# Performance work log

Hardware: AMD Instinct MI355X
Metric: run time of the kernel (lower is better)

Reference implementation:

```python
import jax, jax.numpy as jnp
import numpy as np
from jax import lax

PATCH = 16
DILATIONS = (1, 2, 4, 8)
R2_THRESH = 0.5


def setup_inputs() -> dict:
    key = jax.random.key(0)
    k1, k2, k3 = jax.random.split(key, 3)
    seasonal = jax.random.normal(k1, (32, 2048, 8), dtype=jnp.float32)
    # 4 Conv1d(1,1,k=16) kernels + biases (PyTorch default init scale ~1/sqrt(k))
    conv_w = jax.random.normal(k2, (4, PATCH), dtype=jnp.float32) / np.sqrt(PATCH).astype(np.float32)
    conv_b = jax.random.normal(k3, (4,), dtype=jnp.float32) * 0.01
    return {"seasonal": seasonal, "conv_w": conv_w, "conv_b": conv_b}


def _r2(y):
    n = y.shape[-1]
    x = jnp.arange(n, dtype=y.dtype)
    xm = x - x.mean()                                  # [2p]
    ym = y - y.mean(axis=-1, keepdims=True)            # [..., 2p]
    sxy = jnp.einsum('...k,k->...', ym, xm)
    sxx = jnp.sum(xm * xm)
    syy = jnp.sum(ym * ym, axis=-1)
    return (sxy * sxy) / (sxx * syy)


def _forward(seasonal, conv_w, conv_b):
    B, S, C = seasonal.shape
    p = PATCH
    # channels are processed independently with the SAME convs -> fuse B and C
    x = seasonal.transpose(0, 2, 1).reshape(B * C, 1, S)  # [BC,1,S]
    win = jnp.arange(S - p + 1)[:, None] + jnp.arange(p)[None, :]  # [n_patches,p]
    cand_list = []
    for i, d in enumerate(DILATIONS):
        pad = (p - 1) * d
        out = lax.conv_general_dilated(
            x, conv_w[i].reshape(1, 1, p), window_strides=(1,),
            padding=[(pad, pad)], rhs_dilation=(d,)) + conv_b[i]
        out = out[:, 0, :S]                      # crop to seq_len, [BC,S]
        cand_list.append(out[:, win])            # sliding windows [BC,n_patches,p]
    cand = jnp.concatenate(cand_list, axis=1)    # [BC,N,p]
    N = cand.shape[1]

    # r^2 score for every adjacent pair (vectorized; greedy scan only gates it)
    pair = jnp.concatenate([cand[:, :-1], cand[:, 1:]], axis=-1)  # [BC,N-1,2p]
    can_merge = jnp.pad(_r2(pair) >= R2_THRESH, ((0, 0), (0, 1)),
                        constant_values=False)   # [BC,N]; last idx never merges

    # greedy sequential merge: if pair (i,i+1) merges, i+1 is consumed
    def step(consumed, cm_i):
        merge = jnp.logical_and(~consumed, cm_i)
        return merge, (merge, ~consumed)

    def scan_one(cm):
        _, (merge, valid) = lax.scan(step, jnp.zeros((), jnp.bool_), cm)
        return merge, valid

    merge, valid = jax.vmap(scan_one)(can_merge)  # [BC,N] each

    nxt = jnp.concatenate([cand[:, 1:], cand[:, -1:]], axis=1)
    outs = jnp.where(merge[..., None], 0.5 * (cand + nxt), cand)  # [BC,N,p]

    # pack selected patches to the front (stable order), zero-pad the tail
    order = jnp.argsort(~valid, axis=1)  # jax argsort is stable; valid first
    packed = jnp.take_along_axis(outs, order[..., None], axis=1)
    vmask = jnp.take_along_axis(valid, order, axis=1)
    packed = packed * vmask[..., None].astype(packed.dtype)

    return packed.reshape(B, C, N, p).transpose(0, 2, 3, 1)  # [B,N,p,C]


def reference(seasonal, conv_w, conv_b):
    return _forward(seasonal, conv_w, conv_b)
```

## Files before the change

### kernel.cpp

```cpp
#include <hip/hip_runtime.h>

#define SLEN 2048
#define PATCH 16
#define ND 4
#define NW 2033
#define NCAND 8132
#define NROWS 256
#define NCH 8
#define ROWPAD 8192


__global__ __launch_bounds__(256) void k_conv(
    const float* __restrict__ seasonal,
    const float* __restrict__ conv_w,
    const float* __restrict__ conv_b,
    double* __restrict__ convd,
    float* __restrict__ convf)
{
    const int bid = blockIdx.x;
    const int row = bid >> 2;
    const int d   = bid & 3;
    const int dil = 1 << d;
    const int b = row >> 3, c = row & 7;

    __shared__ float xs[SLEN];
    #pragma unroll
    for (int j = 0; j < SLEN/256; ++j) {
        int s = threadIdx.x + j*256;
        xs[s] = seasonal[(size_t)(b*SLEN + s)*NCH + c];
    }
    double w[PATCH];
    #pragma unroll
    for (int k = 0; k < PATCH; ++k) w[k] = (double)conv_w[d*PATCH + k];
    const double bias = (double)conv_b[d];
    __syncthreads();

    const size_t obase = ((size_t)row*ND + d)*SLEN;
    #pragma unroll
    for (int j = 0; j < SLEN/256; ++j) {
        int t = threadIdx.x + j*256;
        double acc = 0.0;
        #pragma unroll
        for (int k = 0; k < PATCH; ++k) {
            int idx = t - (PATCH-1-k)*dil;
            if (idx >= 0) acc += w[k] * (double)xs[idx];
        }
        acc += bias;
        convd[obase + t] = acc;
        convf[obase + t] = (float)acc;
    }
}

__global__ __launch_bounds__(256) void k_cm(
    const double* __restrict__ convd,
    unsigned char* __restrict__ cmb)
{
    const int row = blockIdx.x >> 2;
    const int d   = blockIdx.x & 3;
    const int tid = threadIdx.x;
    const double* g = convd + ((size_t)row*ND + d)*SLEN;
    unsigned char* crow = cmb + (size_t)row*ROWPAD + d*NW;

    if (tid < 254) {
        const int w0 = tid*8;
        double W1=0.0, W2=0.0, Wk=0.0;
        #pragma unroll
        for (int k = 0; k < 16; ++k) {
            double v = g[w0+k];
            W1 += v; W2 = fma(v,v,W2); Wk = fma((double)k,v,Wk);
        }
        unsigned char bits[8];
        #pragma unroll
        for (int j = 0; j < 8; ++j) {
            double v0 = g[w0+j], v16 = g[w0+j+16];
            double nW1 = W1 + (v16 - v0);
            double nW2 = W2 + (v16*v16 - v0*v0);
            double nWk = Wk - W1 + v0 + 15.0*v16;
            double S1  = W1 + nW1;
            double S2  = W2 + nW2;
            double Sxy = (Wk - 15.5*W1) + (nWk + 0.5*nW1);
            double syy = S2 - S1*S1*(1.0/32.0);
            bits[j] = (unsigned char)((Sxy*Sxy >= 1364.0*syy) && (syy > 0.0));
            W1 = nW1; W2 = nW2; Wk = nWk;
        }
        #pragma unroll
        for (int j = 0; j < 8; ++j) crow[w0+j] = bits[j];
    } else if (tid == 254 && d < 3) {
        const double* g2 = convd + ((size_t)row*ND + d + 1)*SLEN;
        double aW1=0,aW2=0,aWk=0, bW1=0,bW2=0,bWk=0;
        #pragma unroll
        for (int k = 0; k < 16; ++k) {
            double va = g[2032+k]; aW1 += va; aW2 = fma(va,va,aW2); aWk = fma((double)k,va,aWk);
            double vb = g2[k];     bW1 += vb; bW2 = fma(vb,vb,bW2); bWk = fma((double)k,vb,bWk);
        }
        double S1  = aW1 + bW1;
        double S2  = aW2 + bW2;
        double Sxy = (aWk - 15.5*aW1) + (bWk + 0.5*bW1);
        double syy = S2 - S1*S1*(1.0/32.0);
        crow[2032] = (unsigned char)((Sxy*Sxy >= 1364.0*syy) && (syy > 0.0));
    }
}

__global__ __launch_bounds__(256) void k_pack(
    const unsigned char* __restrict__ cmb,
    int* __restrict__ sel)
{
    const int row = blockIdx.x;
    const int tid = threadIdx.x;
    __shared__ unsigned char c0out[256];
    __shared__ int pmax[256];
    __shared__ unsigned sums[256];

    const unsigned* cmw = (const unsigned*)(cmb + (size_t)row*ROWPAD);
    unsigned cmbits = 0;
    #pragma unroll
    for (int q = 0; q < 8; ++q) {
        unsigned wrd = cmw[tid*8 + q];
        #pragma unroll
        for (int bb = 0; bb < 4; ++bb) {
            int p = tid*32 + q*4 + bb;
            unsigned bit = ((wrd >> (8*bb)) & 0xffu) ? 1u : 0u;
            if (p >= NCAND-1) bit = 0;
            cmbits |= bit << (q*4 + bb);
        }
    }

    unsigned inv = ~cmbits;
    unsigned T = (inv == 0u) ? 32u : (unsigned)__clz(inv);
    c0out[tid] = (unsigned char)(T & 1u);
    pmax[tid]  = (inv == 0u) ? -1 : tid;
    __syncthreads();
    for (int off = 1; off < 256; off <<= 1) {
        int v = (tid >= off) ? pmax[tid-off] : -1;
        __syncthreads();
        if (v > pmax[tid]) pmax[tid] = v;
        __syncthreads();
    }
    unsigned carry = 0;
    if (tid > 0) { int m = pmax[tid-1]; if (m >= 0) carry = c0out[m]; }

    unsigned cons = carry;
    unsigned validb = 0, mergeb = 0;
    int cnt = 0;
    const int base = tid*32;
    int nelem = NCAND - base; if (nelem > 32) nelem = 32; if (nelem < 0) nelem = 0;
    for (int w = 0; w < nelem; ++w) {
        unsigned bit = (cmbits >> w) & 1u;
        unsigned val = cons ^ 1u;
        unsigned mrg = bit & val;
        validb |= val << w;
        mergeb |= mrg << w;
        cnt += (int)val;
        cons = mrg;
    }

    sums[tid] = (unsigned)cnt;
    __syncthreads();
    for (int off = 1; off < 256; off <<= 1) {
        unsigned v = (tid >= off) ? sums[tid-off] : 0u;
        __syncthreads();
        sums[tid] += v;
        __syncthreads();
    }
    unsigned r = sums[tid] - (unsigned)cnt;
    unsigned total = sums[255];
    int* selrow = sel + (size_t)row*ROWPAD;
    for (int w = 0; w < nelem; ++w) {
        if ((validb >> w) & 1u)
            selrow[r++] = ((base + w) << 1) | (int)((mergeb >> w) & 1u);
    }
    for (int idx = (int)total + tid; idx < ROWPAD; idx += 256)
        selrow[idx] = -1;
}

__global__ __launch_bounds__(256) void k_out(
    const float* __restrict__ convf,
    const int* __restrict__ sel,
    float* __restrict__ out)
{
    __shared__ float gbuf[8*132];
    __shared__ int   amin_s[8], amax_s[8];
    __shared__ float tile[32*132];

    const int t = threadIdx.x;
    const int c = t & 7;
    const int s = t >> 3;
    const unsigned bq = blockIdx.x;
    const unsigned b  = bq / 255u;
    const unsigned m  = bq - b*255u;
    const int n0 = (int)m*32;
    const int ns = (NCAND - n0 < 32) ? (NCAND - n0) : 32;
    const unsigned row = b*NCH + (unsigned)c;

    if (t < 8) { amin_s[t] = 0x7fffffff; amax_s[t] = -1; }
    __syncthreads();

    int e = -1, ai = 0, ai2 = 0;
    if (s < ns) {
        e = sel[(size_t)row*ROWPAD + (n0 + s)];
        if (e >= 0) {
            const int i  = e >> 1;
            const int d  = (i >= 3*NW) ? 3 : (i >= 2*NW) ? 2 : (i >= NW) ? 1 : 0;
            ai = i + 15*d;
            int ae;
            if (e & 1) {
                const int i2 = i + 1;
                const int d2 = (i2 >= 3*NW) ? 3 : (i2 >= 2*NW) ? 2 : (i2 >= NW) ? 1 : 0;
                ai2 = i2 + 15*d2;
                ae = ai2 + 16;
            } else {
                ai2 = ai;
                ae = ai + 16;
            }
            atomicMin(&amin_s[c], ai);
            atomicMax(&amax_s[c], ae);
        }
    }
    __syncthreads();

    {
        const int r = t >> 5, j = t & 31;
        const int lo = amin_s[r], hi = amax_s[r];
        if (lo <= hi) {
            const float* src = convf + (size_t)(b*NCH + r)*8192;
            for (int o = j; o <= hi - lo; o += 32)
                gbuf[r*132 + o] = src[lo + o];
        }
    }
    __syncthreads();

    float vals[16];
    if (e < 0) {
        #pragma unroll
        for (int k = 0; k < 16; ++k) vals[k] = 0.0f;
    } else {
        const float* f = gbuf + c*132 + (ai  - amin_s[c]);
        const float* g = gbuf + c*132 + (ai2 - amin_s[c]);
        if (e & 1) {
            #pragma unroll
            for (int k = 0; k < 16; ++k) vals[k] = 0.5f*(f[k] + g[k]);
        } else {
            #pragma unroll
            for (int k = 0; k < 16; ++k) vals[k] = f[k];
        }
    }
    if (s < ns) {
        float* tr = tile + s*132 + c;
        #pragma unroll
        for (int k = 0; k < 16; ++k) tr[k*8] = vals[k];
    }
    __syncthreads();

    const size_t obase = ((size_t)b*NCAND + n0)*128;
    const int nw = ns*128;
    #pragma unroll
    for (int m2 = 0; m2 < 4; ++m2) {
        int L = (t + m2*256)*4;
        if (L < nw) {
            int s2 = L >> 7, j = L & 127;
            float4 v = *(const float4*)&tile[s2*132 + j];
            *(float4*)&out[obase + L] = v;
        }
    }
}

extern "C" void kernel_launch(void* const* d_in, const int* in_sizes, int n_in,
                              void* d_out, int out_size, void* d_ws, size_t ws_size,
                              hipStream_t stream) {
    const float* seasonal = (const float*)d_in[0];
    const float* conv_w   = (const float*)d_in[1];
    const float* conv_b   = (const float*)d_in[2];
    float* out = (float*)d_out;

    char* ws = (char*)d_ws;
    double*        convd = (double*)(ws);
    float*         convf = (float*)(ws + 16777216);
    unsigned char* cmb   = (unsigned char*)(ws + 25165824);
    int*           sel   = (int*)(ws);

    hipLaunchKernelGGL(k_conv, dim3(NROWS*ND), dim3(256), 0, stream,
                       seasonal, conv_w, conv_b, convd, convf);
    hipLaunchKernelGGL(k_cm,   dim3(NROWS*ND), dim3(256), 0, stream,
                       convd, cmb);
    hipLaunchKernelGGL(k_pack, dim3(NROWS), dim3(256), 0, stream,
                       cmb, sel);
    hipLaunchKernelGGL(k_out,  dim3(32*255), dim3(256), 0, stream,
                       convf, sel, out);
}
```

Baseline: 174.7 us.

## Fuse conv and merge-test kernels via shared memory, shrink selection indices to 16-bit

Merges the convolution and r^2 merge-test kernels into one. The double-precision conv output now stays in padded shared memory instead of making a round trip through global memory. The cross-dilation boundary pair recomputes the next dilation's first 16 outputs locally. Selection indices become 16-bit and the tail fill stops at NCAND, which cuts k_pack writes and k_out reads. In exchange the kernel holds about 17KB of double shared memory per block, which may lower occupancy, and one thread does extra serial work.

```diff
diff --git a/kernel.cpp b/kernel.cpp
--- a/kernel.cpp
+++ b/kernel.cpp
@@ -10,23 +10,28 @@
 #define ROWPAD 8192
 
 
-__global__ __launch_bounds__(256) void k_conv(
+#define CDX(x) ((x) + ((x) >> 4))
+
+__global__ __launch_bounds__(256) void k_convcm(
     const float* __restrict__ seasonal,
     const float* __restrict__ conv_w,
     const float* __restrict__ conv_b,
-    double* __restrict__ convd,
-    float* __restrict__ convf)
+    float* __restrict__ convf,
+    unsigned char* __restrict__ cmb)
 {
     const int bid = blockIdx.x;
     const int row = bid >> 2;
     const int d   = bid & 3;
     const int dil = 1 << d;
     const int b = row >> 3, c = row & 7;
+    const int tid = threadIdx.x;
 
     __shared__ float xs[SLEN];
+    __shared__ double cd[CDX(SLEN-1)+1];
+
     #pragma unroll
     for (int j = 0; j < SLEN/256; ++j) {
-        int s = threadIdx.x + j*256;
+        int s = tid + j*256;
         xs[s] = seasonal[(size_t)(b*SLEN + s)*NCH + c];
     }
     double w[PATCH];
@@ -35,10 +40,10 @@
     const double bias = (double)conv_b[d];
     __syncthreads();
 
-    const size_t obase = ((size_t)row*ND + d)*SLEN;
+    const size_t obase = (size_t)row*8192 + d*SLEN;
     #pragma unroll
     for (int j = 0; j < SLEN/256; ++j) {
-        int t = threadIdx.x + j*256;
+        int t = tid + j*256;
         double acc = 0.0;
         #pragma unroll
         for (int k = 0; k < PATCH; ++k) {
@@ -46,33 +51,24 @@
             if (idx >= 0) acc += w[k] * (double)xs[idx];
         }
         acc += bias;
-        convd[obase + t] = acc;
+        cd[CDX(t)] = acc;
         convf[obase + t] = (float)acc;
     }
-}
-
-__global__ __launch_bounds__(256) void k_cm(
-    const double* __restrict__ convd,
-    unsigned char* __restrict__ cmb)
-{
-    const int row = blockIdx.x >> 2;
-    const int d   = blockIdx.x & 3;
-    const int tid = threadIdx.x;
-    const double* g = convd + ((size_t)row*ND + d)*SLEN;
+    __syncthreads();
+
     unsigned char* crow = cmb + (size_t)row*ROWPAD + d*NW;
-
     if (tid < 254) {
         const int w0 = tid*8;
         double W1=0.0, W2=0.0, Wk=0.0;
         #pragma unroll
         for (int k = 0; k < 16; ++k) {
-            double v = g[w0+k];
+            double v = cd[CDX(w0+k)];
             W1 += v; W2 = fma(v,v,W2); Wk = fma((double)k,v,Wk);
         }
         unsigned char bits[8];
         #pragma unroll
         for (int j = 0; j < 8; ++j) {
-            double v0 = g[w0+j], v16 = g[w0+j+16];
+            double v0 = cd[CDX(w0+j)], v16 = cd[CDX(w0+j+16)];
             double nW1 = W1 + (v16 - v0);
             double nW2 = W2 + (v16*v16 - v0*v0);
             double nWk = Wk - W1 + v0 + 15.0*v16;
@@ -85,13 +81,25 @@
         }
         #pragma unroll
         for (int j = 0; j < 8; ++j) crow[w0+j] = bits[j];
-    } else if (tid == 254 && d < 3) {
-        const double* g2 = convd + ((size_t)row*ND + d + 1)*SLEN;
+    } else if (tid == 255 && d < 3) {
+        const int dil2 = dil << 1;
+        double w2[PATCH];
+        #pragma unroll
+        for (int k = 0; k < PATCH; ++k) w2[k] = (double)conv_w[(d+1)*PATCH + k];
+        const double bias2 = (double)conv_b[d+1];
         double aW1=0,aW2=0,aWk=0, bW1=0,bW2=0,bWk=0;
         #pragma unroll
         for (int k = 0; k < 16; ++k) {
-            double va = g[2032+k]; aW1 += va; aW2 = fma(va,va,aW2); aWk = fma((double)k,va,aWk);
-            double vb = g2[k];     bW1 += vb; bW2 = fma(vb,vb,bW2); bWk = fma((double)k,vb,bWk);
+            double va = cd[CDX(2032+k)];
+            double acc = 0.0;
+            #pragma unroll
+            for (int q = 0; q < PATCH; ++q) {
+                int idx = k - (PATCH-1-q)*dil2;
+                if (idx >= 0) acc += w2[q] * (double)xs[idx];
+            }
+            double vb = acc + bias2;
+            aW1 += va; aW2 = fma(va,va,aW2); aWk = fma((double)k,va,aWk);
+            bW1 += vb; bW2 = fma(vb,vb,bW2); bWk = fma((double)k,vb,bWk);
         }
         double S1  = aW1 + bW1;
         double S2  = aW2 + bW2;
@@ -103,7 +111,7 @@
 
 __global__ __launch_bounds__(256) void k_pack(
     const unsigned char* __restrict__ cmb,
-    int* __restrict__ sel)
+    unsigned short* __restrict__ sel)
 {
     const int row = blockIdx.x;
     const int tid = threadIdx.x;
@@ -164,18 +172,18 @@
     }
     unsigned r = sums[tid] - (unsigned)cnt;
     unsigned total = sums[255];
-    int* selrow = sel + (size_t)row*ROWPAD;
+    unsigned short* selrow = sel + (size_t)row*ROWPAD;
     for (int w = 0; w < nelem; ++w) {
         if ((validb >> w) & 1u)
-            selrow[r++] = ((base + w) << 1) | (int)((mergeb >> w) & 1u);
-    }
-    for (int idx = (int)total + tid; idx < ROWPAD; idx += 256)
-        selrow[idx] = -1;
+            selrow[r++] = (unsigned short)((((base + w) << 1) | (int)((mergeb >> w) & 1u)));
+    }
+    for (int idx = (int)total + tid; idx < NCAND; idx += 256)
+        selrow[idx] = 0xFFFFu;
 }
 
 __global__ __launch_bounds__(256) void k_out(
     const float* __restrict__ convf,
-    const int* __restrict__ sel,
+    const unsigned short* __restrict__ sel,
     float* __restrict__ out)
 {
     __shared__ float gbuf[8*132];
@@ -197,7 +205,8 @@
 
     int e = -1, ai = 0, ai2 = 0;
     if (s < ns) {
-        e = sel[(size_t)row*ROWPAD + (n0 + s)];
+        unsigned short e16 = sel[(size_t)row*ROWPAD + (n0 + s)];
+        e = (e16 == 0xFFFFu) ? -1 : (int)e16;
         if (e >= 0) {
             const int i  = e >> 1;
             const int d  = (i >= 3*NW) ? 3 : (i >= 2*NW) ? 2 : (i >= NW) ? 1 : 0;
@@ -273,17 +282,14 @@
     float* out = (float*)d_out;
 
     char* ws = (char*)d_ws;
-    double*        convd = (double*)(ws);
-    float*         convf = (float*)(ws + 16777216);
-    unsigned char* cmb   = (unsigned char*)(ws + 25165824);
-    int*           sel   = (int*)(ws);
-
-    hipLaunchKernelGGL(k_conv, dim3(NROWS*ND), dim3(256), 0, stream,
-                       seasonal, conv_w, conv_b, convd, convf);
-    hipLaunchKernelGGL(k_cm,   dim3(NROWS*ND), dim3(256), 0, stream,
-                       convd, cmb);
-    hipLaunchKernelGGL(k_pack, dim3(NROWS), dim3(256), 0, stream,
+    unsigned short* sel   = (unsigned short*)(ws);
+    float*          convf = (float*)(ws + 16777216);
+    unsigned char*  cmb   = (unsigned char*)(ws + 25165824);
+
+    hipLaunchKernelGGL(k_convcm, dim3(NROWS*ND), dim3(256), 0, stream,
+                       seasonal, conv_w, conv_b, convf, cmb);
+    hipLaunchKernelGGL(k_pack,   dim3(NROWS), dim3(256), 0, stream,
                        cmb, sel);
-    hipLaunchKernelGGL(k_out,  dim3(32*255), dim3(256), 0, stream,
+    hipLaunchKernelGGL(k_out,    dim3(32*255), dim3(256), 0, stream,
                        convf, sel, out);
 }
```

Measured after the change: 169.2 us, median of 2. 1.03x faster.
